# Kernel tuning notes

Measured on AMD Instinct MI355X. Metric: run time of the kernel, lower is better.

Reference implementation:

```python
import jax, jax.numpy as jnp
import numpy as np
import math

WINDOW_SIZE = 11
SIGMA = 1.5

def _gaussian_window(window_size, channel):
    g = np.array([math.exp(-(x - window_size // 2) ** 2 / (2 * SIGMA ** 2)) for x in range(window_size)], dtype=np.float32)
    g = g / g.sum()
    w2d = np.outer(g, g).astype(np.float32)  # [K,K]
    # depthwise kernel, OIHW with O=channel, I=1
    return jnp.asarray(np.broadcast_to(w2d, (channel, 1, window_size, window_size)).copy())

def _dwconv(x, window):
    # x: [B,C,H,W], window: [C,1,K,K]; 'same' padding depthwise conv
    pad = WINDOW_SIZE // 2
    return jax.lax.conv_general_dilated(
        x, window, window_strides=(1, 1), padding=[(pad, pad), (pad, pad)],
        feature_group_count=x.shape[1],
        dimension_numbers=('NCHW', 'OIHW', 'NCHW'))

def setup_inputs() -> dict:
    key = jax.random.key(0)
    k1, k2 = jax.random.split(key)
    pred = jax.random.uniform(k1, (16, 3, 512, 512), dtype=jnp.float32)
    label = jax.random.uniform(k2, (16, 3, 512, 512), dtype=jnp.float32)
    return {"pred": pred, "label": label}

def reference(pred, label):
    img1, img2 = pred, label
    channel = img1.shape[1]
    window = _gaussian_window(WINDOW_SIZE, channel)
    mu1 = _dwconv(img1, window)
    mu2 = _dwconv(img2, window)
    mu1_sq = mu1 * mu1
    mu2_sq = mu2 * mu2
    mu1_mu2 = mu1 * mu2
    sigma1_sq = _dwconv(img1 * img1, window) - mu1_sq
    sigma2_sq = _dwconv(img2 * img2, window) - mu2_sq
    sigma12 = _dwconv(img1 * img2, window) - mu1_mu2
    C1, C2 = 0.01 ** 2, 0.03 ** 2
    ssim_map = ((2 * mu1_mu2 + C1) * (2 * sigma12 + C2)) / ((mu1_sq + mu2_sq + C1) * (sigma1_sq + sigma2_sq + C2))
    return 1.0 - ssim_map.mean()
```

## Files before the change

kernel.cpp:

```cpp
#include <hip/hip_runtime.h>

#define IMG_W 512
#define IMG_H 512
#define NPLANES 48
#define NPIX 12582912.0
#define CST 44
#define FSZ (32 * CST)
#define NBLOCKS (16*16*48)


__global__ __launch_bounds__(256) void ssim_fused_kernel(
    const float* __restrict__ pred,
    const float* __restrict__ label,
    float* __restrict__ partial)
{
    __shared__ float hT[5 * FSZ];

    const int tid = threadIdx.x;
    const int ox = blockIdx.x * 32;
    const int oy = blockIdx.y * 32;
    const int plane = blockIdx.z;
    const float* __restrict__ xp = pred  + (size_t)plane * (IMG_W * IMG_H);
    const float* __restrict__ yp = label + (size_t)plane * (IMG_W * IMG_H);

    float w[11];
    {
        float s = 0.f;
        #pragma unroll
        for (int i = 0; i < 11; ++i) {
            float d = (float)(i - 5);
            w[i] = expf(-d * d / 4.5f);
            s += w[i];
        }
        float inv = 1.0f / s;
        #pragma unroll
        for (int i = 0; i < 11; ++i) w[i] *= inv;
    }

    const bool xInterior = (blockIdx.x != 0) && (blockIdx.x != (IMG_W / 32 - 1));
    for (int i = tid; i < 336; i += 256) {
        int r  = i >> 3;
        int g  = i & 7;
        int gy = oy - 5 + r;
        int c0 = ox + g * 4;

        float bx_[24], by_[24];
        bool rowok = ((unsigned)gy < (unsigned)IMG_H);
        if (!rowok) {
            #pragma unroll
            for (int j = 0; j < 24; ++j) { bx_[j] = 0.f; by_[j] = 0.f; }
        } else if (xInterior) {
            const float4* px4 = reinterpret_cast<const float4*>(xp + gy * IMG_W + (c0 - 8));
            const float4* py4 = reinterpret_cast<const float4*>(yp + gy * IMG_W + (c0 - 8));
            #pragma unroll
            for (int j = 0; j < 6; ++j) {
                float4 a = px4[j];
                float4 b = py4[j];
                bx_[4*j+0] = a.x; bx_[4*j+1] = a.y; bx_[4*j+2] = a.z; bx_[4*j+3] = a.w;
                by_[4*j+0] = b.x; by_[4*j+1] = b.y; by_[4*j+2] = b.z; by_[4*j+3] = b.w;
            }
        } else {
            #pragma unroll
            for (int j = 0; j < 24; ++j) {
                int col = c0 - 8 + j;
                bool ok = ((unsigned)col < (unsigned)IMG_W);
                bx_[j] = ok ? xp[gy * IMG_W + col] : 0.f;
                by_[j] = ok ? yp[gy * IMG_W + col] : 0.f;
            }
        }

        float a0[4] = {0,0,0,0}, a1[4] = {0,0,0,0}, a2[4] = {0,0,0,0},
              a3[4] = {0,0,0,0}, a4[4] = {0,0,0,0};
        #pragma unroll
        for (int j = 3; j <= 16; ++j) {
            float xv = bx_[j], yv = by_[j];
            float xx = xv * xv, yy = yv * yv, xy = xv * yv;
            #pragma unroll
            for (int o = 0; o < 4; ++o) {
                int k = j - 3 - o;
                if (k >= 0 && k <= 10) {
                    float wk = w[k];
                    a0[o] += wk * xv;
                    a1[o] += wk * yv;
                    a2[o] += wk * xx;
                    a3[o] += wk * yy;
                    a4[o] += wk * xy;
                }
            }
        }

        int wb = g * (4 * CST) + r;
        #pragma unroll
        for (int o = 0; o < 4; ++o) {
            hT[wb + o*CST + 0*FSZ] = a0[o];
            hT[wb + o*CST + 1*FSZ] = a1[o];
            hT[wb + o*CST + 2*FSZ] = a2[o];
            hT[wb + o*CST + 3*FSZ] = a3[o];
            hT[wb + o*CST + 4*FSZ] = a4[o];
        }
    }
    __syncthreads();

    float lsum = 0.f;
    {
        int c  = tid & 31;
        int rg = tid >> 5;
        int d  = c * CST + 4 * rg;

        float m[5][4];
        #pragma unroll
        for (int f = 0; f < 5; ++f) {
            const float4* p = reinterpret_cast<const float4*>(&hT[f*FSZ + d]);
            float4 v0 = p[0], v1 = p[1], v2 = p[2], v3 = p[3];
            float vv[16] = { v0.x, v0.y, v0.z, v0.w,
                             v1.x, v1.y, v1.z, v1.w,
                             v2.x, v2.y, v2.z, v2.w,
                             v3.x, v3.y, v3.z, v3.w };
            #pragma unroll
            for (int o = 0; o < 4; ++o) {
                float s = 0.f;
                #pragma unroll
                for (int k = 0; k < 11; ++k) s += w[k] * vv[o + k];
                m[f][o] = s;
            }
        }

        #pragma unroll
        for (int o = 0; o < 4; ++o) {
            float mu1 = m[0][o], mu2 = m[1][o];
            float mu1s = mu1 * mu1, mu2s = mu2 * mu2, mu12 = mu1 * mu2;
            float s1  = m[2][o] - mu1s;
            float s2  = m[3][o] - mu2s;
            float s12 = m[4][o] - mu12;
            const float C1 = 1e-4f, C2 = 9e-4f;
            float num = (2.f * mu12 + C1) * (2.f * s12 + C2);
            float den = (mu1s + mu2s + C1) * (s1 + s2 + C2);
            lsum += num * __builtin_amdgcn_rcpf(den);
        }
    }

    #pragma unroll
    for (int off = 32; off > 0; off >>= 1)
        lsum += __shfl_down(lsum, off, 64);

    __shared__ float wsum[4];
    if ((tid & 63) == 0) wsum[tid >> 6] = lsum;
    __syncthreads();
    if (tid == 0) {
        int bid = (blockIdx.z * gridDim.y + blockIdx.y) * gridDim.x + blockIdx.x;
        partial[bid] = wsum[0] + wsum[1] + wsum[2] + wsum[3];
    }
}

__global__ __launch_bounds__(1024) void ssim_finalize_kernel(
    const float* __restrict__ partial, float* __restrict__ out)
{
    double s = 0.0;
    for (int i = threadIdx.x; i < NBLOCKS; i += 1024) s += (double)partial[i];
    #pragma unroll
    for (int off = 32; off > 0; off >>= 1) s += __shfl_down(s, off, 64);
    __shared__ double ws[16];
    if ((threadIdx.x & 63) == 0) ws[threadIdx.x >> 6] = s;
    __syncthreads();
    if (threadIdx.x == 0) {
        double t = 0.0;
        #pragma unroll
        for (int k = 0; k < 16; ++k) t += ws[k];
        out[0] = 1.0f - (float)(t * (1.0 / NPIX));
    }
}

extern "C" void kernel_launch(void* const* d_in, const int* in_sizes, int n_in,
                              void* d_out, int out_size, void* d_ws, size_t ws_size,
                              hipStream_t stream) {
    const float* pred  = (const float*)d_in[0];
    const float* label = (const float*)d_in[1];
    float* out = (float*)d_out;
    float* partial = (float*)d_ws;

    dim3 grid(IMG_W / 32, IMG_H / 32, NPLANES);
    ssim_fused_kernel<<<grid, 256, 0, stream>>>(pred, label, partial);
    ssim_finalize_kernel<<<1, 1024, 0, stream>>>(partial, out);
}
```

Before: 180.7 us.

## Compute vertical Gaussian pass with bf16 MFMA on banded weight matrix

```diff
diff --git a/kernel.cpp b/kernel.cpp
--- a/kernel.cpp
+++ b/kernel.cpp
@@ -4,9 +4,18 @@
 #define IMG_H 512
 #define NPLANES 48
 #define NPIX 12582912.0
-#define CST 44
-#define FSZ (32 * CST)
+#define SB 72
+#define FSB (32 * SB)
 #define NBLOCKS (16*16*48)
+
+typedef __attribute__((ext_vector_type(8))) short bf16x8;
+typedef __attribute__((ext_vector_type(4))) float f32x4;
+
+static __device__ inline unsigned short f2bf(float v) {
+    union { float f; unsigned int u; } x; x.f = v;
+    unsigned int r = x.u + 0x7FFFu + ((x.u >> 16) & 1u);
+    return (unsigned short)(r >> 16);
+}
 
 
 __global__ __launch_bounds__(256) void ssim_fused_kernel(
@@ -14,7 +23,7 @@
     const float* __restrict__ label,
     float* __restrict__ partial)
 {
-    __shared__ float hT[5 * FSZ];
+    __shared__ unsigned short hB[5 * FSB];
 
     const int tid = threadIdx.x;
     const int ox = blockIdx.x * 32;
@@ -38,100 +47,123 @@
     }
 
     const bool xInterior = (blockIdx.x != 0) && (blockIdx.x != (IMG_W / 32 - 1));
-    for (int i = tid; i < 336; i += 256) {
+    for (int i = tid; i < 512; i += 256) {
         int r  = i >> 3;
         int g  = i & 7;
-        int gy = oy - 5 + r;
-        int c0 = ox + g * 4;
-
-        float bx_[24], by_[24];
-        bool rowok = ((unsigned)gy < (unsigned)IMG_H);
-        if (!rowok) {
+        int wb = (g * 4) * SB + r;
+        if (r < 42) {
+            int gy = oy - 5 + r;
+            int c0 = ox + g * 4;
+
+            float bx_[24], by_[24];
+            bool rowok = ((unsigned)gy < (unsigned)IMG_H);
+            if (!rowok) {
+                #pragma unroll
+                for (int j = 0; j < 24; ++j) { bx_[j] = 0.f; by_[j] = 0.f; }
+            } else if (xInterior) {
+                const float4* px4 = reinterpret_cast<const float4*>(xp + gy * IMG_W + (c0 - 8));
+                const float4* py4 = reinterpret_cast<const float4*>(yp + gy * IMG_W + (c0 - 8));
+                #pragma unroll
+                for (int j = 0; j < 6; ++j) {
+                    float4 a = px4[j];
+                    float4 b = py4[j];
+                    bx_[4*j+0] = a.x; bx_[4*j+1] = a.y; bx_[4*j+2] = a.z; bx_[4*j+3] = a.w;
+                    by_[4*j+0] = b.x; by_[4*j+1] = b.y; by_[4*j+2] = b.z; by_[4*j+3] = b.w;
+                }
+            } else {
+                #pragma unroll
+                for (int j = 0; j < 24; ++j) {
+                    int col = c0 - 8 + j;
+                    bool ok = ((unsigned)col < (unsigned)IMG_W);
+                    bx_[j] = ok ? xp[gy * IMG_W + col] : 0.f;
+                    by_[j] = ok ? yp[gy * IMG_W + col] : 0.f;
+                }
+            }
+
+            float a0[4] = {0,0,0,0}, a1[4] = {0,0,0,0}, a2[4] = {0,0,0,0},
+                  a3[4] = {0,0,0,0}, a4[4] = {0,0,0,0};
             #pragma unroll
-            for (int j = 0; j < 24; ++j) { bx_[j] = 0.f; by_[j] = 0.f; }
-        } else if (xInterior) {
-            const float4* px4 = reinterpret_cast<const float4*>(xp + gy * IMG_W + (c0 - 8));
-            const float4* py4 = reinterpret_cast<const float4*>(yp + gy * IMG_W + (c0 - 8));
+            for (int j = 3; j <= 16; ++j) {
+                float xv = bx_[j], yv = by_[j];
+                float xx = xv * xv, yy = yv * yv, xy = xv * yv;
+                #pragma unroll
+                for (int o = 0; o < 4; ++o) {
+                    int k = j - 3 - o;
+                    if (k >= 0 && k <= 10) {
+                        float wk = w[k];
+                        a0[o] += wk * xv;
+                        a1[o] += wk * yv;
+                        a2[o] += wk * xx;
+                        a3[o] += wk * yy;
+                        a4[o] += wk * xy;
+                    }
+                }
+            }
             #pragma unroll
-            for (int j = 0; j < 6; ++j) {
-                float4 a = px4[j];
-                float4 b = py4[j];
-                bx_[4*j+0] = a.x; bx_[4*j+1] = a.y; bx_[4*j+2] = a.z; bx_[4*j+3] = a.w;
-                by_[4*j+0] = b.x; by_[4*j+1] = b.y; by_[4*j+2] = b.z; by_[4*j+3] = b.w;
+            for (int o = 0; o < 4; ++o) {
+                hB[wb + o*SB + 0*FSB] = f2bf(a0[o]);
+                hB[wb + o*SB + 1*FSB] = f2bf(a1[o]);
+                hB[wb + o*SB + 2*FSB] = f2bf(a2[o]);
+                hB[wb + o*SB + 3*FSB] = f2bf(a3[o]);
+                hB[wb + o*SB + 4*FSB] = f2bf(a4[o]);
             }
         } else {
             #pragma unroll
-            for (int j = 0; j < 24; ++j) {
-                int col = c0 - 8 + j;
-                bool ok = ((unsigned)col < (unsigned)IMG_W);
-                bx_[j] = ok ? xp[gy * IMG_W + col] : 0.f;
-                by_[j] = ok ? yp[gy * IMG_W + col] : 0.f;
-            }
-        }
-
-        float a0[4] = {0,0,0,0}, a1[4] = {0,0,0,0}, a2[4] = {0,0,0,0},
-              a3[4] = {0,0,0,0}, a4[4] = {0,0,0,0};
-        #pragma unroll
-        for (int j = 3; j <= 16; ++j) {
-            float xv = bx_[j], yv = by_[j];
-            float xx = xv * xv, yy = yv * yv, xy = xv * yv;
-            #pragma unroll
             for (int o = 0; o < 4; ++o) {
-                int k = j - 3 - o;
-                if (k >= 0 && k <= 10) {
-                    float wk = w[k];
-                    a0[o] += wk * xv;
-                    a1[o] += wk * yv;
-                    a2[o] += wk * xx;
-                    a3[o] += wk * yy;
-                    a4[o] += wk * xy;
-                }
-            }
-        }
-
-        int wb = g * (4 * CST) + r;
-        #pragma unroll
-        for (int o = 0; o < 4; ++o) {
-            hT[wb + o*CST + 0*FSZ] = a0[o];
-            hT[wb + o*CST + 1*FSZ] = a1[o];
-            hT[wb + o*CST + 2*FSZ] = a2[o];
-            hT[wb + o*CST + 3*FSZ] = a3[o];
-            hT[wb + o*CST + 4*FSZ] = a4[o];
+                hB[wb + o*SB + 0*FSB] = 0;
+                hB[wb + o*SB + 1*FSB] = 0;
+                hB[wb + o*SB + 2*FSB] = 0;
+                hB[wb + o*SB + 3*FSB] = 0;
+                hB[wb + o*SB + 4*FSB] = 0;
+            }
         }
     }
     __syncthreads();
 
     float lsum = 0.f;
     {
-        int c  = tid & 31;
-        int rg = tid >> 5;
-        int d  = c * CST + 4 * rg;
-
-        float m[5][4];
+        const int lane = tid & 63;
+        const int wid  = tid >> 6;
+        const int R    = wid >> 1;
+        const int Cc   = wid & 1;
+        const int lrow = lane & 15;
+        const int lk   = (lane >> 4) << 3;
+
+        bf16x8 afr0, afr1;
+        #pragma unroll
+        for (int j = 0; j < 8; ++j) {
+            int m0 = lk + j;
+            int i0 = m0 - (16 * R + lrow);
+            float v0 = (i0 >= 0 && i0 <= 10) ? w[i0] : 0.f;
+            afr0[j] = (short)f2bf(v0);
+            int m1 = m0 + 32;
+            int i1 = m1 - (16 * R + lrow);
+            float v1 = (i1 >= 0 && i1 <= 10) ? w[i1] : 0.f;
+            afr1[j] = (short)f2bf(v1);
+        }
+
+        const int bcol = (16 * Cc + lrow) * SB + lk;
+
+        f32x4 acc[5];
         #pragma unroll
         for (int f = 0; f < 5; ++f) {
-            const float4* p = reinterpret_cast<const float4*>(&hT[f*FSZ + d]);
-            float4 v0 = p[0], v1 = p[1], v2 = p[2], v3 = p[3];
-            float vv[16] = { v0.x, v0.y, v0.z, v0.w,
-                             v1.x, v1.y, v1.z, v1.w,
-                             v2.x, v2.y, v2.z, v2.w,
-                             v3.x, v3.y, v3.z, v3.w };
-            #pragma unroll
-            for (int o = 0; o < 4; ++o) {
-                float s = 0.f;
-                #pragma unroll
-                for (int k = 0; k < 11; ++k) s += w[k] * vv[o + k];
-                m[f][o] = s;
-            }
-        }
-
-        #pragma unroll
-        for (int o = 0; o < 4; ++o) {
-            float mu1 = m[0][o], mu2 = m[1][o];
+            f32x4 a = {0.f, 0.f, 0.f, 0.f};
+            bf16x8 b0 = *reinterpret_cast<const bf16x8*>(&hB[f * FSB + bcol]);
+            a = __builtin_amdgcn_mfma_f32_16x16x32_bf16(afr0, b0, a, 0, 0, 0);
+            if (R == 1) {
+                bf16x8 b1 = *reinterpret_cast<const bf16x8*>(&hB[f * FSB + bcol + 32]);
+                a = __builtin_amdgcn_mfma_f32_16x16x32_bf16(afr1, b1, a, 0, 0, 0);
+            }
+            acc[f] = a;
+        }
+
+        #pragma unroll
+        for (int i = 0; i < 4; ++i) {
+            float mu1 = acc[0][i], mu2 = acc[1][i];
             float mu1s = mu1 * mu1, mu2s = mu2 * mu2, mu12 = mu1 * mu2;
-            float s1  = m[2][o] - mu1s;
-            float s2  = m[3][o] - mu2s;
-            float s12 = m[4][o] - mu12;
+            float s1  = acc[2][i] - mu1s;
+            float s2  = acc[3][i] - mu2s;
+            float s12 = acc[4][i] - mu12;
             const float C1 = 1e-4f, C2 = 9e-4f;
             float num = (2.f * mu12 + C1) * (2.f * s12 + C2);
             float den = (mu1s + mu2s + C1) * (s1 + s2 + C2);
```

Measured after the change: 188.8 us. +4.5%, slower.
